# Performance work log

Hardware: AMD Instinct MI355X
Metric: run time of the kernel (lower is better)

## Reference

```python
import jax, jax.numpy as jnp
import numpy as np

RES = 192      # resolution
RANK = 8       # low-rank
FD = 32        # feature_dim
NFPD = 32      # num_features_per_dim = round(32768**(1/3))
RADIUS = 1.3
NI = 128       # n_intersections
STEP = 0.0352  # step_size
B = 2048       # rays


def setup_inputs():
    key = jax.random.key(0)
    ks = jax.random.split(key, 12)
    ro = jax.random.normal(ks[0], (B, 3), dtype=jnp.float32)
    ro = ro / jnp.linalg.norm(ro, axis=-1, keepdims=True) * 2.5  # origins outside the cube
    rd = -ro + 0.1 * jax.random.normal(ks[1], (B, 3), dtype=jnp.float32)
    rd = rd / jnp.linalg.norm(rd, axis=-1, keepdims=True)        # roughly toward origin
    def nrm(k, shape, std):
        return std * jax.random.normal(k, shape, dtype=jnp.float32)
    return {
        "rays_o": ro, "rays_d": rd,
        "Gxy": nrm(ks[2], (RES, RES, 3, RANK), 0.1),
        "Gxz": nrm(ks[3], (RES, RES, 3, RANK), 0.1),
        "Gyz": nrm(ks[4], (RES, RES, 3, RANK), 0.1),
        "F_grid": nrm(ks[5], (NFPD, NFPD, NFPD, FD), 0.05),
        "sW0": nrm(ks[6], (FD, 128), FD ** -0.5),
        "sW1": nrm(ks[7], (128, 128), 128 ** -0.5),
        "sW2": nrm(ks[8], (128, 16), 128 ** -0.5),
        "cW0": nrm(ks[9], (31, 64), 31 ** -0.5),
        "cW1": nrm(ks[10], (64, 64), 64 ** -0.5),
        "cW2": nrm(ks[11], (64, 3), 64 ** -0.5),
    }


def trilinear(vol, coords):
    # vol: [D,H,W,C]; coords: [N,3] as (x,y,z) in [-1,1]; x indexes W (last spatial dim)
    # matches torch grid_sample(align_corners=True, mode='bilinear', padding_mode='border')
    D, H, W, C = vol.shape
    def prep(c, size):
        idx = jnp.clip((c + 1.0) * 0.5 * (size - 1), 0.0, size - 1.0)  # border clamp
        i0 = jnp.clip(jnp.floor(idx).astype(jnp.int32), 0, size - 2)
        return i0, i0 + 1, idx - i0
    x0, x1, wx = prep(coords[:, 0], W)
    y0, y1, wy = prep(coords[:, 1], H)
    z0, z1, wz = prep(coords[:, 2], D)
    wx = wx[:, None]; wy = wy[:, None]; wz = wz[:, None]
    def g(zi, yi, xi):
        return vol[zi, yi, xi]  # [N,C]
    c00 = g(z0, y0, x0) * (1 - wx) + g(z0, y0, x1) * wx
    c01 = g(z0, y1, x0) * (1 - wx) + g(z0, y1, x1) * wx
    c10 = g(z1, y0, x0) * (1 - wx) + g(z1, y0, x1) * wx
    c11 = g(z1, y1, x0) * (1 - wx) + g(z1, y1, x1) * wx
    c0 = c00 * (1 - wy) + c01 * wy
    c1 = c10 * (1 - wy) + c11 * wy
    return c0 * (1 - wz) + c1 * wz


def sh16(d):
    # tcnn SphericalHarmonics degree 4 on directions (input (d+1)/2 is unmapped back to d internally)
    x, y, z = d[:, 0], d[:, 1], d[:, 2]
    x2, y2, z2 = x * x, y * y, z * z
    return jnp.stack([
        jnp.full_like(x, 0.28209479177387814),
        -0.48860251190291987 * y,
        0.48860251190291987 * z,
        -0.48860251190291987 * x,
        1.0925484305920792 * x * y,
        -1.0925484305920792 * y * z,
        0.94617469575755997 * z2 - 0.31539156525251999,
        -1.0925484305920792 * x * z,
        0.54627421529603959 * (x2 - y2),
        0.59004358992664352 * y * (-3.0 * x2 + y2),
        2.8906114426405538 * x * y * z,
        0.45704579946446572 * y * (1.0 - 5.0 * z2),
        0.3731763325901154 * z * (5.0 * z2 - 3.0),
        0.45704579946446572 * x * (1.0 - 5.0 * z2),
        1.445305721320277 * z * (x2 - y2),
        0.59004358992664352 * x * (-x2 + 3.0 * y2),
    ], axis=-1)


def _forward(rays_o, rays_d, Gxy, Gxz, Gyz, F_grid, sW0, sW1, sW2, cW0, cW1, cW2):
    b = rays_o.shape[0]
    # --- get_intersections: ray/AABB [-R,R]^3, uniform marching ---
    d = jnp.where(jnp.abs(rays_d) < 1e-9, 1e-9, rays_d)
    t1 = (-RADIUS - rays_o) / d
    t2 = (RADIUS - rays_o) / d
    tmin = jnp.max(jnp.minimum(t1, t2), axis=-1)
    tmax = jnp.min(jnp.maximum(t1, t2), axis=-1)
    near = jnp.maximum(tmin, 0.0)
    ts = near[:, None] + jnp.arange(NI + 1, dtype=jnp.float32) * STEP  # intersections [B,NI+1]
    tmid = 0.5 * (ts[:, :-1] + ts[:, 1:])                              # [B,NI]
    pts = rays_o[:, None, :] + tmid[..., None] * rays_d[:, None, :]    # [B,NI,3]
    mask = (jnp.all(jnp.abs(pts) <= RADIUS, axis=-1)
            & (tmid <= tmax[:, None]) & (tmax > tmin)[:, None])        # [B,NI]
    rdn = rays_d / jnp.linalg.norm(rays_d, axis=-1, keepdims=True)
    # coordinate chain of forward + eval_pts nets out to pts/RADIUS in [-1,1]
    p = ((pts / RADIUS + 1.0) * RES / 2.0) * 2.0 / RES - 1.0
    pf = p.reshape(-1, 3)
    # --- densify low-rank tri-plane grid: sum_r Gxy*Gxz*Gyz -> [RES,RES,RES,3] ---
    grid = jnp.zeros((RES, RES, RES, 3), dtype=Gxy.dtype)
    for r in range(RANK):  # fixed small rank; avoids a [RES^3,3,RANK] intermediate
        grid = grid + (Gxy[:, :, None, :, r] * Gxz[:, None, :, :, r] * Gyz[None, :, :, :, r])
    # --- eval_pts: grid_sample -> hash-feature grid_sample -> MLPs ---
    Gvals = trilinear(grid, pf)            # [N,3]
    Fvals = trilinear(F_grid, Gvals)       # [N,FD]
    h = jax.nn.relu(Fvals @ sW0)
    h = jax.nn.relu(h @ sW1)
    out16 = h @ sW2                        # [N,16]
    sigma = out16[:, 0].reshape(b, NI)
    sigma = jax.nn.relu(jnp.where(mask, sigma, 0.0))
    rdn_pts = jnp.broadcast_to(rdn[:, None, :], (b, NI, 3)).reshape(-1, 3)
    ci = jnp.concatenate([sh16(rdn_pts), out16[:, 1:]], axis=-1)  # [N,31]
    c = jax.nn.relu(ci @ cW0)
    c = jax.nn.relu(c @ cW1)
    color = (c @ cW2).reshape(b, NI, 3)
    color = jnp.where(mask[..., None], color, 0.0)
    # --- sigma2alpha + shrgb2rgb (white background) ---
    dists = ts[:, 1:] - ts[:, :-1]         # |rdn| == 1
    alpha = 1.0 - jnp.exp(-sigma * dists)
    T = jnp.cumprod(1.0 - alpha + 1e-10, axis=-1)
    T = jnp.concatenate([jnp.ones_like(T[:, :1]), T[:, :-1]], axis=-1)  # exclusive
    w = alpha * T                          # abs_light [B,NI]
    rgb = jax.nn.sigmoid(color)
    acc = jnp.sum(w, axis=-1)
    return jnp.sum(w[..., None] * rgb, axis=1) + (1.0 - acc)[..., None]  # [B,3]


def reference(rays_o, rays_d, Gxy, Gxz, Gyz, F_grid, sW0, sW1, sW2, cW0, cW1, cW2):
    return _forward(rays_o, rays_d, Gxy, Gxz, Gyz, F_grid, sW0, sW1, sW2, cW0, cW1, cW2)
```

## Files before the change

kernel.cpp:

```cpp
#include <hip/hip_runtime.h>
#include <math.h>

#define RES 192
#define RANK 8
#define NI 128
#define LW 136

typedef __attribute__((ext_vector_type(8))) _Float16 h8;
typedef __attribute__((ext_vector_type(2))) _Float16 h2f;
typedef __attribute__((ext_vector_type(4))) float floatx4;

#define OFF_SW0 0
#define OFF_SW1 4096
#define OFF_SW2 20480
#define OFF_CW0 22528
#define OFF_CW1 24576
#define OFF_CW2 28672
#define PACK_TOTAL 29696

#define TRI_CELLS (RES*RES)
#define TRI_TOTAL (3*TRI_CELLS*24)
#define FG_TOTAL  (32*32*32*32)
#define PREP_TOTAL (PACK_TOTAL + TRI_TOTAL + FG_TOTAL)

__device__ __forceinline__ void prep_idx(float c, int size, int& i0, float& f){
    float idx = (c + 1.0f)*0.5f*(float)(size-1);
    idx = fminf(fmaxf(idx, 0.0f), (float)(size-1));
    int ii = (int)idx;
    if (ii > size-2) ii = size-2;
    i0 = ii;
    f = idx - (float)ii;
}

__device__ __forceinline__ float wred64(float v){
    #pragma unroll
    for (int o=32;o>0;o>>=1) v += __shfl_down(v, o, 64);
    return v;
}

__device__ __forceinline__ h8 shx1(h8 v){
    union { h8 h; int i[4]; } u; u.h = v;
    #pragma unroll
    for (int k=0;k<4;k++) u.i[k] = __shfl_xor(u.i[k], 1, 64);
    return u.h;
}

__global__ void __launch_bounds__(256) prep_all(
    const float* __restrict__ sW0, const float* __restrict__ sW1,
    const float* __restrict__ sW2, const float* __restrict__ cW0,
    const float* __restrict__ cW1, const float* __restrict__ cW2,
    const float* __restrict__ Gxy, const float* __restrict__ Gxz,
    const float* __restrict__ Gyz, const float* __restrict__ F_grid,
    _Float16* __restrict__ Wp, _Float16* __restrict__ Gp, _Float16* __restrict__ Fg)
{
    int e = blockIdx.x*256 + threadIdx.x;
    if (e < PACK_TOTAL){
        const float* src; int K, N, ksteps, base;
        if      (e < OFF_SW1){ src=sW0; K=32;  N=128; ksteps=1; base=OFF_SW0; }
        else if (e < OFF_SW2){ src=sW1; K=128; N=128; ksteps=4; base=OFF_SW1; }
        else if (e < OFF_CW0){ src=sW2; K=128; N=16;  ksteps=4; base=OFF_SW2; }
        else if (e < OFF_CW1){ src=cW0; K=31;  N=64;  ksteps=1; base=OFF_CW0; }
        else if (e < OFF_CW2){ src=cW1; K=64;  N=64;  ksteps=2; base=OFF_CW1; }
        else                 { src=cW2; K=64;  N=3;   ksteps=2; base=OFF_CW2; }
        int i = e - base;
        int j = i & 7, lane = (i>>3)&63, t = i>>9;
        int ks = t % ksteps, nt = t / ksteps;
        int k = ks*32 + (lane>>4)*8 + j;
        int n = nt*16 + (lane&15);
        float v = (k < K && n < N) ? src[k*N + n] : 0.0f;
        Wp[e] = (_Float16)v;
        return;
    }
    int e2 = e - PACK_TOTAL;
    if (e2 < TRI_TOTAL){
        int p    = e2 / (TRI_CELLS*24);
        int rem  = e2 - p*(TRI_CELLS*24);
        int cell = rem / 24;
        int c    = rem - cell*24;
        const float* src = (p==0) ? Gxy : (p==1) ? Gxz : Gyz;
        Gp[((size_t)(p*TRI_CELLS + cell))*32 + c] = (_Float16)src[(size_t)cell*24 + c];
        return;
    }
    int e3 = e2 - TRI_TOTAL;
    Fg[e3] = (_Float16)F_grid[e3];
}

__launch_bounds__(256, 4)
__global__ void nerf_fused(
    const float* __restrict__ rays_o, const float* __restrict__ rays_d,
    const _Float16* __restrict__ Gp, const _Float16* __restrict__ Fg,
    const _Float16* __restrict__ Wp, float* __restrict__ out)
{
    __shared__ _Float16 buf[128*LW];
    __shared__ float sigmaArr[128];
    __shared__ float rgbArr[128*3];
    __shared__ float wtot[2];
    __shared__ float partial[8];

    const int tid  = threadIdx.x;
    const int lane = tid & 63;
    const int wv   = tid >> 6;
    const int ray  = blockIdx.x;

    const int rowbase = wv*32;
    const int col  = lane & 15;
    const int quad = lane >> 4;
    const int ar0  = rowbase + col;
    const int ar1  = ar0 + 16;

    const float ox = rays_o[ray*3+0], oy = rays_o[ray*3+1], oz = rays_o[ray*3+2];
    const float dx = rays_d[ray*3+0], dy = rays_d[ray*3+1], dz = rays_d[ray*3+2];

    float sdx = (fabsf(dx) < 1e-9f) ? 1e-9f : dx;
    float sdy = (fabsf(dy) < 1e-9f) ? 1e-9f : dy;
    float sdz = (fabsf(dz) < 1e-9f) ? 1e-9f : dz;
    float t1x = (-1.3f - ox)/sdx, t2x = (1.3f - ox)/sdx;
    float t1y = (-1.3f - oy)/sdy, t2y = (1.3f - oy)/sdy;
    float t1z = (-1.3f - oz)/sdz, t2z = (1.3f - oz)/sdz;
    float tmin = fmaxf(fminf(t1x,t2x), fmaxf(fminf(t1y,t2y), fminf(t1z,t2z)));
    float tmax = fminf(fmaxf(t1x,t2x), fminf(fmaxf(t1y,t2y), fmaxf(t1z,t2z)));
    float nearv = fmaxf(tmin, 0.0f);

    bool skipAll;
    {
        int sid = rowbase + (lane & 31);
        float w_ts0 = nearv + (float)sid     * 0.0352f;
        float w_ts1 = nearv + (float)(sid+1) * 0.0352f;
        float w_tm  = 0.5f*(w_ts0+w_ts1);
        float wpx = ox + w_tm*dx, wpy = oy + w_tm*dy, wpz = oz + w_tm*dz;
        bool m = (fabsf(wpx)<=1.3f) && (fabsf(wpy)<=1.3f) && (fabsf(wpz)<=1.3f)
               && (w_tm<=tmax) && (tmax>tmin);
        skipAll = (__ballot(m) == 0ULL);
    }

    if (!skipAll){
        {
            const int s = rowbase + (lane >> 1);
            const int h = lane & 1;

            float ts0 = nearv + (float)s     * 0.0352f;
            float ts1 = nearv + (float)(s+1) * 0.0352f;
            float tmid = 0.5f*(ts0+ts1);
            float px = ox + tmid*dx, py = oy + tmid*dy, pz = oz + tmid*dz;
            bool mask = (fabsf(px)<=1.3f) && (fabsf(py)<=1.3f) && (fabsf(pz)<=1.3f)
                      && (tmid<=tmax) && (tmax>tmin);

            h8 FVa = {0,0,0,0,0,0,0,0};
            h8 FVb = {0,0,0,0,0,0,0,0};

            if (mask){
                float p0 = (px/1.3f + 1.0f)*192.0f/2.0f*2.0f/192.0f - 1.0f;
                float p1 = (py/1.3f + 1.0f)*192.0f/2.0f*2.0f/192.0f - 1.0f;
                float p2 = (pz/1.3f + 1.0f)*192.0f/2.0f*2.0f/192.0f - 1.0f;

                int x0, y0, z0; float fx, fy, fz;
                prep_idx(p0, RES, x0, fx);
                prep_idx(p1, RES, y0, fy);
                prep_idx(p2, RES, z0, fz);

                const int zi  = z0 + h;
                const float wzc = h ? fz : (1.0f - fz);
                const int yiA = y0 + h;
                const int yiB = y0 + 1 - h;

                h8 XYA[3], XYB[3], XZ0[3], XZ1[3], YZo0[3], YZo1[3];
                {
                    const h8* pxyA = (const h8*)(Gp + ((size_t)(zi*RES + yiA))*32);
                    const h8* pxyB = (const h8*)(Gp + ((size_t)(zi*RES + yiB))*32);
                    const h8* px0  = (const h8*)(Gp + ((size_t)(TRI_CELLS + zi*RES + x0  ))*32);
                    const h8* px1  = (const h8*)(Gp + ((size_t)(TRI_CELLS + zi*RES + x0+1))*32);
                    const h8* py0  = (const h8*)(Gp + ((size_t)(2*TRI_CELLS + yiA*RES + x0  ))*32);
                    const h8* py1  = (const h8*)(Gp + ((size_t)(2*TRI_CELLS + yiA*RES + x0+1))*32);
                    #pragma unroll
                    for (int q=0;q<3;q++){
                        XYA[q]=pxyA[q]; XYB[q]=pxyB[q];
                        XZ0[q]=px0[q];  XZ1[q]=px1[q];
                        YZo0[q]=py0[q]; YZo1[q]=py1[q];
                    }
                }
                h8 YZp0[3], YZp1[3];
                #pragma unroll
                for (int q=0;q<3;q++){ YZp0[q]=shx1(YZo0[q]); YZp1[q]=shx1(YZo1[q]); }

                const float wyA = h ? fy : (1.0f - fy);
                const float wyB = h ? (1.0f - fy) : fy;

                h8 ACC0 = {0,0,0,0,0,0,0,0};
                h8 ACC1 = {0,0,0,0,0,0,0,0};
                h8 ACC2 = {0,0,0,0,0,0,0,0};
                #pragma unroll
                for (int yo=0; yo<2; yo++){
                    const float wy = yo ? wyB : wyA;
                    #pragma unroll
                    for (int xc=0; xc<2; xc++){
                        const float wx = xc ? fx : (1.0f - fx);
                        const _Float16 wh = (_Float16)(wzc*wy*wx);
                        const h8 w8 = {wh,wh,wh,wh,wh,wh,wh,wh};
                        h8 Q0, Q1, Q2;
                        if (yo==0){
                            const h8* YZv = xc ? YZo1 : YZo0;
                            Q0 = (XYA[0]*(xc?XZ1[0]:XZ0[0]))*YZv[0];
                            Q1 = (XYA[1]*(xc?XZ1[1]:XZ0[1]))*YZv[1];
                            Q2 = (XYA[2]*(xc?XZ1[2]:XZ0[2]))*YZv[2];
                        } else {
                            const h8* YZv = xc ? YZp1 : YZp0;
                            Q0 = (XYB[0]*(xc?XZ1[0]:XZ0[0]))*YZv[0];
                            Q1 = (XYB[1]*(xc?XZ1[1]:XZ0[1]))*YZv[1];
                            Q2 = (XYB[2]*(xc?XZ1[2]:XZ0[2]))*YZv[2];
                        }
                        ACC0 = __builtin_elementwise_fma(Q0, w8, ACC0);
                        ACC1 = __builtin_elementwise_fma(Q1, w8, ACC1);
                        ACC2 = __builtin_elementwise_fma(Q2, w8, ACC2);
                    }
                }
                h2f a0h = __builtin_shufflevector(ACC0,ACC0,0,1) + __builtin_shufflevector(ACC0,ACC0,2,3);
                h2f b0h = __builtin_shufflevector(ACC0,ACC0,4,5) + __builtin_shufflevector(ACC0,ACC0,6,7);
                h2f c0h = a0h + b0h;
                float gv0 = (float)c0h[0] + (float)c0h[1];
                h2f a1h = __builtin_shufflevector(ACC1,ACC1,0,1) + __builtin_shufflevector(ACC1,ACC1,2,3);
                h2f b1h = __builtin_shufflevector(ACC1,ACC1,4,5) + __builtin_shufflevector(ACC1,ACC1,6,7);
                h2f c1h = a1h + b1h;
                float gv1 = (float)c1h[0] + (float)c1h[1];
                h2f a2h = __builtin_shufflevector(ACC2,ACC2,0,1) + __builtin_shufflevector(ACC2,ACC2,2,3);
                h2f b2h = __builtin_shufflevector(ACC2,ACC2,4,5) + __builtin_shufflevector(ACC2,ACC2,6,7);
                h2f c2h = a2h + b2h;
                float gv2 = (float)c2h[0] + (float)c2h[1];

                gv0 += __shfl_xor(gv0, 1, 64);
                gv1 += __shfl_xor(gv1, 1, 64);
                gv2 += __shfl_xor(gv2, 1, 64);

                int a0,b0,c0; float fa,fb,fc;
                prep_idx(gv2, 32, a0, fa);
                prep_idx(gv1, 32, b0, fb);
                prep_idx(gv0, 32, c0, fc);
                #pragma unroll
                for (int zc=0; zc<2; zc++){
                    const int zi2 = a0+zc; const float wz2 = zc ? fa : 1.f-fa;
                    #pragma unroll
                    for (int yc=0; yc<2; yc++){
                        const int yi2 = b0+yc; const float wy2 = yc ? fb : 1.f-fb;
                        #pragma unroll
                        for (int xc=0; xc<2; xc++){
                            const int xi2 = c0+xc; const float wx2 = xc ? fc : 1.f-fc;
                            const _Float16 wh = (_Float16)(wz2*wy2*wx2);
                            const h8 w8 = {wh,wh,wh,wh,wh,wh,wh,wh};
                            const h8* pf = (const h8*)(Fg + ((size_t)((zi2*32+yi2)*32+xi2))*32 + h*16);
                            FVa = __builtin_elementwise_fma(pf[0], w8, FVa);
                            FVb = __builtin_elementwise_fma(pf[1], w8, FVb);
                        }
                    }
                }
            }

            *(h8*)&buf[s*LW + h*16]     = FVa;
            *(h8*)&buf[s*LW + h*16 + 8] = FVb;
        }

        {
            h8 a0 = *(const h8*)&buf[ar0*LW + quad*8];
            h8 a1 = *(const h8*)&buf[ar1*LW + quad*8];
            const h8* W = (const h8*)(Wp + OFF_SW0);
            #pragma unroll
            for (int nt=0; nt<8; nt++){
                h8 b = W[nt*64 + lane];
                floatx4 c0v = {0.f,0.f,0.f,0.f}, c1v = {0.f,0.f,0.f,0.f};
                c0v = __builtin_amdgcn_mfma_f32_16x16x32_f16(a0, b, c0v, 0,0,0);
                c1v = __builtin_amdgcn_mfma_f32_16x16x32_f16(a1, b, c1v, 0,0,0);
                #pragma unroll
                for (int r=0;r<4;r++){
                    int row0 = rowbase + quad*4 + r;
                    buf[row0*LW      + nt*16 + col] = (_Float16)fmaxf(c0v[r],0.f);
                    buf[(row0+16)*LW + nt*16 + col] = (_Float16)fmaxf(c1v[r],0.f);
                }
            }
        }

        {
            h8 A0[4], A1[4];
            #pragma unroll
            for (int ks=0;ks<4;ks++){
                A0[ks] = *(const h8*)&buf[ar0*LW + ks*32 + quad*8];
                A1[ks] = *(const h8*)&buf[ar1*LW + ks*32 + quad*8];
            }
            const h8* W = (const h8*)(Wp + OFF_SW1);
            #pragma unroll
            for (int nt=0; nt<8; nt++){
                floatx4 c0v = {0.f,0.f,0.f,0.f}, c1v = {0.f,0.f,0.f,0.f};
                #pragma unroll
                for (int ks=0;ks<4;ks++){
                    h8 b = W[(nt*4+ks)*64 + lane];
                    c0v = __builtin_amdgcn_mfma_f32_16x16x32_f16(A0[ks], b, c0v, 0,0,0);
                    c1v = __builtin_amdgcn_mfma_f32_16x16x32_f16(A1[ks], b, c1v, 0,0,0);
                }
                #pragma unroll
                for (int r=0;r<4;r++){
                    int row0 = rowbase + quad*4 + r;
                    buf[row0*LW      + nt*16 + col] = (_Float16)fmaxf(c0v[r],0.f);
                    buf[(row0+16)*LW + nt*16 + col] = (_Float16)fmaxf(c1v[r],0.f);
                }
            }
        }

        {
            h8 A0[4], A1[4];
            #pragma unroll
            for (int ks=0;ks<4;ks++){
                A0[ks] = *(const h8*)&buf[ar0*LW + ks*32 + quad*8];
                A1[ks] = *(const h8*)&buf[ar1*LW + ks*32 + quad*8];
            }
            const h8* W = (const h8*)(Wp + OFF_SW2);
            floatx4 c0v = {0.f,0.f,0.f,0.f}, c1v = {0.f,0.f,0.f,0.f};
            #pragma unroll
            for (int ks=0;ks<4;ks++){
                h8 b = W[ks*64 + lane];
                c0v = __builtin_amdgcn_mfma_f32_16x16x32_f16(A0[ks], b, c0v, 0,0,0);
                c1v = __builtin_amdgcn_mfma_f32_16x16x32_f16(A1[ks], b, c1v, 0,0,0);
            }
            #pragma unroll
            for (int r=0;r<4;r++){
                int row0 = rowbase + quad*4 + r;
                if (col == 0){
                    sigmaArr[row0]    = c0v[r];
                    sigmaArr[row0+16] = c1v[r];
                } else {
                    buf[row0*LW      + 15 + col] = (_Float16)c0v[r];
                    buf[(row0+16)*LW + 15 + col] = (_Float16)c1v[r];
                }
            }
            const float dn = sqrtf(dx*dx+dy*dy+dz*dz);
            const float X = dx/dn, Y = dy/dn, Z = dz/dn;
            const float X2=X*X, Y2=Y*Y, Z2=Z*Z;
            float sh[16];
            sh[0]= 0.28209479177387814f;
            sh[1]=-0.48860251190291987f*Y;
            sh[2]= 0.48860251190291987f*Z;
            sh[3]=-0.48860251190291987f*X;
            sh[4]= 1.0925484305920792f*X*Y;
            sh[5]=-1.0925484305920792f*Y*Z;
            sh[6]= 0.94617469575756f*Z2 - 0.31539156525252f;
            sh[7]=-1.0925484305920792f*X*Z;
            sh[8]= 0.5462742152960396f*(X2-Y2);
            sh[9]= 0.5900435899266435f*Y*(-3.0f*X2+Y2);
            sh[10]=2.890611442640554f*X*Y*Z;
            sh[11]=0.4570457994644657f*Y*(1.0f-5.0f*Z2);
            sh[12]=0.3731763325901154f*Z*(5.0f*Z2-3.0f);
            sh[13]=0.4570457994644657f*X*(1.0f-5.0f*Z2);
            sh[14]=1.445305721320277f*Z*(X2-Y2);
            sh[15]=0.5900435899266435f*X*(-X2+3.0f*Y2);
            if (lane < 32){
                int row = rowbase + lane;
                #pragma unroll
                for (int k=0;k<16;k++) buf[row*LW + k] = (_Float16)sh[k];
            }
        }

        {
            h8 a0 = *(const h8*)&buf[ar0*LW + quad*8];
            h8 a1 = *(const h8*)&buf[ar1*LW + quad*8];
            const h8* W = (const h8*)(Wp + OFF_CW0);
            #pragma unroll
            for (int nt=0; nt<4; nt++){
                h8 b = W[nt*64 + lane];
                floatx4 c0v = {0.f,0.f,0.f,0.f}, c1v = {0.f,0.f,0.f,0.f};
                c0v = __builtin_amdgcn_mfma_f32_16x16x32_f16(a0, b, c0v, 0,0,0);
                c1v = __builtin_amdgcn_mfma_f32_16x16x32_f16(a1, b, c1v, 0,0,0);
                #pragma unroll
                for (int r=0;r<4;r++){
                    int row0 = rowbase + quad*4 + r;
                    buf[row0*LW      + nt*16 + col] = (_Float16)fmaxf(c0v[r],0.f);
                    buf[(row0+16)*LW + nt*16 + col] = (_Float16)fmaxf(c1v[r],0.f);
                }
            }
        }

        {
            h8 A0[2], A1[2];
            #pragma unroll
            for (int ks=0;ks<2;ks++){
                A0[ks] = *(const h8*)&buf[ar0*LW + ks*32 + quad*8];
                A1[ks] = *(const h8*)&buf[ar1*LW + ks*32 + quad*8];
            }
            const h8* W = (const h8*)(Wp + OFF_CW1);
            #pragma unroll
            for (int nt=0; nt<4; nt++){
                floatx4 c0v = {0.f,0.f,0.f,0.f}, c1v = {0.f,0.f,0.f,0.f};
                #pragma unroll
                for (int ks=0;ks<2;ks++){
                    h8 b = W[(nt*2+ks)*64 + lane];
                    c0v = __builtin_amdgcn_mfma_f32_16x16x32_f16(A0[ks], b, c0v, 0,0,0);
                    c1v = __builtin_amdgcn_mfma_f32_16x16x32_f16(A1[ks], b, c1v, 0,0,0);
                }
                #pragma unroll
                for (int r=0;r<4;r++){
                    int row0 = rowbase + quad*4 + r;
                    buf[row0*LW      + nt*16 + col] = (_Float16)fmaxf(c0v[r],0.f);
                    buf[(row0+16)*LW + nt*16 + col] = (_Float16)fmaxf(c1v[r],0.f);
                }
            }
        }

        {
            h8 A0[2], A1[2];
            #pragma unroll
            for (int ks=0;ks<2;ks++){
                A0[ks] = *(const h8*)&buf[ar0*LW + ks*32 + quad*8];
                A1[ks] = *(const h8*)&buf[ar1*LW + ks*32 + quad*8];
            }
            const h8* W = (const h8*)(Wp + OFF_CW2);
            floatx4 c0v = {0.f,0.f,0.f,0.f}, c1v = {0.f,0.f,0.f,0.f};
            #pragma unroll
            for (int ks=0;ks<2;ks++){
                h8 b = W[ks*64 + lane];
                c0v = __builtin_amdgcn_mfma_f32_16x16x32_f16(A0[ks], b, c0v, 0,0,0);
                c1v = __builtin_amdgcn_mfma_f32_16x16x32_f16(A1[ks], b, c1v, 0,0,0);
            }
            if (col < 3){
                #pragma unroll
                for (int r=0;r<4;r++){
                    int row0 = rowbase + quad*4 + r;
                    rgbArr[row0*3 + col]      = c0v[r];
                    rgbArr[(row0+16)*3 + col] = c1v[r];
                }
            }
        }
    }

    __syncthreads();

    {
        float alpha = 0.f, rr = 0.f, rg = 0.f, rb = 0.f;
        if (tid < 128){
            float ts0 = nearv + (float)tid     * 0.0352f;
            float ts1 = nearv + (float)(tid+1) * 0.0352f;
            float tmid = 0.5f*(ts0+ts1);
            float dist = ts1 - ts0;
            float px = ox + tmid*dx, py = oy + tmid*dy, pz = oz + tmid*dz;
            bool mask = (fabsf(px)<=1.3f) && (fabsf(py)<=1.3f) && (fabsf(pz)<=1.3f)
                      && (tmid<=tmax) && (tmax>tmin);
            float sg = mask ? fmaxf(sigmaArr[tid], 0.f) : 0.f;
            alpha = 1.0f - expf(-sg*dist);
            if (mask){
                rr = 1.0f/(1.0f+expf(-rgbArr[tid*3+0]));
                rg = 1.0f/(1.0f+expf(-rgbArr[tid*3+1]));
                rb = 1.0f/(1.0f+expf(-rgbArr[tid*3+2]));
            }
        }
        float p = 1.0f - alpha + 1e-10f;
        #pragma unroll
        for (int off=1; off<64; off<<=1){
            float u = __shfl_up(p, off, 64);
            if (lane >= off) p *= u;
        }
        if (tid < 128 && lane == 63) wtot[wv] = p;
        float excl = __shfl_up(p, 1, 64);
        if (lane == 0) excl = 1.0f;
        __syncthreads();
        if (tid < 128){
            float T = excl;
            if (wv == 1) T *= wtot[0];
            float w = alpha * T;
            float v0 = wred64(w*rr);
            float v1 = wred64(w*rg);
            float v2 = wred64(w*rb);
            float v3 = wred64(w);
            if (lane == 0){
                partial[wv*4+0]=v0; partial[wv*4+1]=v1; partial[wv*4+2]=v2; partial[wv*4+3]=v3;
            }
        }
        __syncthreads();
        if (tid == 0){
            float acc = partial[3] + partial[7];
            float bg  = 1.0f - acc;
            out[ray*3+0] = partial[0] + partial[4] + bg;
            out[ray*3+1] = partial[1] + partial[5] + bg;
            out[ray*3+2] = partial[2] + partial[6] + bg;
        }
    }
}

extern "C" void kernel_launch(void* const* d_in, const int* in_sizes, int n_in,
                              void* d_out, int out_size, void* d_ws, size_t ws_size,
                              hipStream_t stream){
    const float* rays_o = (const float*)d_in[0];
    const float* rays_d = (const float*)d_in[1];
    const float* Gxy    = (const float*)d_in[2];
    const float* Gxz    = (const float*)d_in[3];
    const float* Gyz    = (const float*)d_in[4];
    const float* F_grid = (const float*)d_in[5];
    const float* sW0    = (const float*)d_in[6];
    const float* sW1    = (const float*)d_in[7];
    const float* sW2    = (const float*)d_in[8];
    const float* cW0    = (const float*)d_in[9];
    const float* cW1    = (const float*)d_in[10];
    const float* cW2    = (const float*)d_in[11];

    _Float16* Wp = (_Float16*)d_ws;
    _Float16* Gp = Wp + PACK_TOTAL;
    _Float16* Fg = Gp + (size_t)3*TRI_CELLS*32;

    prep_all<<<PREP_TOTAL/256, 256, 0, stream>>>(sW0,sW1,sW2,cW0,cW1,cW2,
                                                 Gxy,Gxz,Gyz,F_grid, Wp,Gp,Fg);
    nerf_fused<<<2048, 256, 0, stream>>>(rays_o, rays_d, Gp, Fg, Wp, (float*)d_out);
}
```

Baseline: 130.7 us.

## Split rays into half-blocks, add separate composite kernel, vectorize weight prep

The fused per-ray kernel is split so each ray is handled by two 128-thread blocks of 64 samples each. Each half exits early on its own when none of its samples fall inside the volume. Per-sample sigma and color go to a workspace buffer, and a new composite kernel does alpha compositing with one wave per ray. The prep kernel now converts factor planes and the feature grid with float4 loads and h8 stores instead of one scalar per thread. The trade-offs are an extra kernel launch and a global round trip for the per-sample outputs.

```diff
diff --git a/kernel.cpp b/kernel.cpp
--- a/kernel.cpp
+++ b/kernel.cpp
@@ -19,9 +19,9 @@
 #define PACK_TOTAL 29696
 
 #define TRI_CELLS (RES*RES)
-#define TRI_TOTAL (3*TRI_CELLS*24)
+#define CELLS3    (3*TRI_CELLS)
 #define FG_TOTAL  (32*32*32*32)
-#define PREP_TOTAL (PACK_TOTAL + TRI_TOTAL + FG_TOTAL)
+#define PREP2_TOTAL (PACK_TOTAL + CELLS3 + FG_TOTAL/8)
 
 __device__ __forceinline__ void prep_idx(float c, int size, int& i0, float& f){
     float idx = (c + 1.0f)*0.5f*(float)(size-1);
@@ -45,7 +45,7 @@
     return u.h;
 }
 
-__global__ void __launch_bounds__(256) prep_all(
+__global__ void __launch_bounds__(256) prep_all2(
     const float* __restrict__ sW0, const float* __restrict__ sW1,
     const float* __restrict__ sW2, const float* __restrict__ cW0,
     const float* __restrict__ cW1, const float* __restrict__ cW2,
@@ -72,35 +72,47 @@
         return;
     }
     int e2 = e - PACK_TOTAL;
-    if (e2 < TRI_TOTAL){
-        int p    = e2 / (TRI_CELLS*24);
-        int rem  = e2 - p*(TRI_CELLS*24);
-        int cell = rem / 24;
-        int c    = rem - cell*24;
-        const float* src = (p==0) ? Gxy : (p==1) ? Gxz : Gyz;
-        Gp[((size_t)(p*TRI_CELLS + cell))*32 + c] = (_Float16)src[(size_t)cell*24 + c];
+    if (e2 < CELLS3){
+        int p, lc;
+        if      (e2 < TRI_CELLS)   { p = 0; lc = e2; }
+        else if (e2 < 2*TRI_CELLS) { p = 1; lc = e2 - TRI_CELLS; }
+        else                       { p = 2; lc = e2 - 2*TRI_CELLS; }
+        const float* src = ((p==0) ? Gxy : (p==1) ? Gxz : Gyz) + (size_t)lc*24;
+        const float4* s4 = (const float4*)src;
+        float4 a = s4[0], b = s4[1], c = s4[2], d = s4[3], ee = s4[4], ff = s4[5];
+        h8 o0 = {(_Float16)a.x,(_Float16)a.y,(_Float16)a.z,(_Float16)a.w,
+                 (_Float16)b.x,(_Float16)b.y,(_Float16)b.z,(_Float16)b.w};
+        h8 o1 = {(_Float16)c.x,(_Float16)c.y,(_Float16)c.z,(_Float16)c.w,
+                 (_Float16)d.x,(_Float16)d.y,(_Float16)d.z,(_Float16)d.w};
+        h8 o2 = {(_Float16)ee.x,(_Float16)ee.y,(_Float16)ee.z,(_Float16)ee.w,
+                 (_Float16)ff.x,(_Float16)ff.y,(_Float16)ff.z,(_Float16)ff.w};
+        h8 zz = {0,0,0,0,0,0,0,0};
+        h8* dst = (h8*)(Gp + (size_t)e2*32);
+        dst[0]=o0; dst[1]=o1; dst[2]=o2; dst[3]=zz;
         return;
     }
-    int e3 = e2 - TRI_TOTAL;
-    Fg[e3] = (_Float16)F_grid[e3];
-}
-
-__launch_bounds__(256, 4)
-__global__ void nerf_fused(
+    int t = e2 - CELLS3;
+    const float4* s4 = (const float4*)(F_grid + (size_t)t*8);
+    float4 a = s4[0], b = s4[1];
+    h8 o = {(_Float16)a.x,(_Float16)a.y,(_Float16)a.z,(_Float16)a.w,
+            (_Float16)b.x,(_Float16)b.y,(_Float16)b.z,(_Float16)b.w};
+    ((h8*)Fg)[t] = o;
+}
+
+__launch_bounds__(128, 4)
+__global__ void nerf_half(
     const float* __restrict__ rays_o, const float* __restrict__ rays_d,
     const _Float16* __restrict__ Gp, const _Float16* __restrict__ Fg,
-    const _Float16* __restrict__ Wp, float* __restrict__ out)
+    const _Float16* __restrict__ Wp, float* __restrict__ SO)
 {
-    __shared__ _Float16 buf[128*LW];
-    __shared__ float sigmaArr[128];
-    __shared__ float rgbArr[128*3];
-    __shared__ float wtot[2];
-    __shared__ float partial[8];
+    __shared__ _Float16 buf[64*LW];
 
     const int tid  = threadIdx.x;
     const int lane = tid & 63;
     const int wv   = tid >> 6;
-    const int ray  = blockIdx.x;
+    const int ray  = blockIdx.x >> 1;
+    const int half = blockIdx.x & 1;
+    const int base = half*64;
 
     const int rowbase = wv*32;
     const int col  = lane & 15;
@@ -123,7 +135,7 @@
 
     bool skipAll;
     {
-        int sid = rowbase + (lane & 31);
+        int sid = base + rowbase + (lane & 31);
         float w_ts0 = nearv + (float)sid     * 0.0352f;
         float w_ts1 = nearv + (float)(sid+1) * 0.0352f;
         float w_tm  = 0.5f*(w_ts0+w_ts1);
@@ -132,350 +144,366 @@
                && (w_tm<=tmax) && (tmax>tmin);
         skipAll = (__ballot(m) == 0ULL);
     }
-
-    if (!skipAll){
-        {
-            const int s = rowbase + (lane >> 1);
-            const int h = lane & 1;
-
-            float ts0 = nearv + (float)s     * 0.0352f;
-            float ts1 = nearv + (float)(s+1) * 0.0352f;
-            float tmid = 0.5f*(ts0+ts1);
-            float px = ox + tmid*dx, py = oy + tmid*dy, pz = oz + tmid*dz;
-            bool mask = (fabsf(px)<=1.3f) && (fabsf(py)<=1.3f) && (fabsf(pz)<=1.3f)
-                      && (tmid<=tmax) && (tmax>tmin);
-
-            h8 FVa = {0,0,0,0,0,0,0,0};
-            h8 FVb = {0,0,0,0,0,0,0,0};
-
-            if (mask){
-                float p0 = (px/1.3f + 1.0f)*192.0f/2.0f*2.0f/192.0f - 1.0f;
-                float p1 = (py/1.3f + 1.0f)*192.0f/2.0f*2.0f/192.0f - 1.0f;
-                float p2 = (pz/1.3f + 1.0f)*192.0f/2.0f*2.0f/192.0f - 1.0f;
-
-                int x0, y0, z0; float fx, fy, fz;
-                prep_idx(p0, RES, x0, fx);
-                prep_idx(p1, RES, y0, fy);
-                prep_idx(p2, RES, z0, fz);
-
-                const int zi  = z0 + h;
-                const float wzc = h ? fz : (1.0f - fz);
-                const int yiA = y0 + h;
-                const int yiB = y0 + 1 - h;
-
-                h8 XYA[3], XYB[3], XZ0[3], XZ1[3], YZo0[3], YZo1[3];
-                {
-                    const h8* pxyA = (const h8*)(Gp + ((size_t)(zi*RES + yiA))*32);
-                    const h8* pxyB = (const h8*)(Gp + ((size_t)(zi*RES + yiB))*32);
-                    const h8* px0  = (const h8*)(Gp + ((size_t)(TRI_CELLS + zi*RES + x0  ))*32);
-                    const h8* px1  = (const h8*)(Gp + ((size_t)(TRI_CELLS + zi*RES + x0+1))*32);
-                    const h8* py0  = (const h8*)(Gp + ((size_t)(2*TRI_CELLS + yiA*RES + x0  ))*32);
-                    const h8* py1  = (const h8*)(Gp + ((size_t)(2*TRI_CELLS + yiA*RES + x0+1))*32);
+    if (skipAll) return;
+
+    {
+        const int s_loc = rowbase + (lane >> 1);
+        const int s_glb = base + s_loc;
+        const int h = lane & 1;
+
+        float ts0 = nearv + (float)s_glb     * 0.0352f;
+        float ts1 = nearv + (float)(s_glb+1) * 0.0352f;
+        float tmid = 0.5f*(ts0+ts1);
+        float px = ox + tmid*dx, py = oy + tmid*dy, pz = oz + tmid*dz;
+        bool mask = (fabsf(px)<=1.3f) && (fabsf(py)<=1.3f) && (fabsf(pz)<=1.3f)
+                  && (tmid<=tmax) && (tmax>tmin);
+
+        h8 FVa = {0,0,0,0,0,0,0,0};
+        h8 FVb = {0,0,0,0,0,0,0,0};
+
+        if (mask){
+            float p0 = (px/1.3f + 1.0f)*192.0f/2.0f*2.0f/192.0f - 1.0f;
+            float p1 = (py/1.3f + 1.0f)*192.0f/2.0f*2.0f/192.0f - 1.0f;
+            float p2 = (pz/1.3f + 1.0f)*192.0f/2.0f*2.0f/192.0f - 1.0f;
+
+            int x0, y0, z0; float fx, fy, fz;
+            prep_idx(p0, RES, x0, fx);
+            prep_idx(p1, RES, y0, fy);
+            prep_idx(p2, RES, z0, fz);
+
+            const int zi  = z0 + h;
+            const float wzc = h ? fz : (1.0f - fz);
+            const int yiA = y0 + h;
+            const int yiB = y0 + 1 - h;
+
+            h8 XYA[3], XYB[3], XZ0[3], XZ1[3], YZo0[3], YZo1[3];
+            {
+                const h8* pxyA = (const h8*)(Gp + ((size_t)(zi*RES + yiA))*32);
+                const h8* pxyB = (const h8*)(Gp + ((size_t)(zi*RES + yiB))*32);
+                const h8* px0  = (const h8*)(Gp + ((size_t)(TRI_CELLS + zi*RES + x0  ))*32);
+                const h8* px1  = (const h8*)(Gp + ((size_t)(TRI_CELLS + zi*RES + x0+1))*32);
+                const h8* py0  = (const h8*)(Gp + ((size_t)(2*TRI_CELLS + yiA*RES + x0  ))*32);
+                const h8* py1  = (const h8*)(Gp + ((size_t)(2*TRI_CELLS + yiA*RES + x0+1))*32);
+                #pragma unroll
+                for (int q=0;q<3;q++){
+                    XYA[q]=pxyA[q]; XYB[q]=pxyB[q];
+                    XZ0[q]=px0[q];  XZ1[q]=px1[q];
+                    YZo0[q]=py0[q]; YZo1[q]=py1[q];
+                }
+            }
+            h8 YZp0[3], YZp1[3];
+            #pragma unroll
+            for (int q=0;q<3;q++){ YZp0[q]=shx1(YZo0[q]); YZp1[q]=shx1(YZo1[q]); }
+
+            const float wyA = h ? fy : (1.0f - fy);
+            const float wyB = h ? (1.0f - fy) : fy;
+
+            h8 ACC0 = {0,0,0,0,0,0,0,0};
+            h8 ACC1 = {0,0,0,0,0,0,0,0};
+            h8 ACC2 = {0,0,0,0,0,0,0,0};
+            #pragma unroll
+            for (int yo=0; yo<2; yo++){
+                const float wy = yo ? wyB : wyA;
+                #pragma unroll
+                for (int xc=0; xc<2; xc++){
+                    const float wx = xc ? fx : (1.0f - fx);
+                    const _Float16 wh = (_Float16)(wzc*wy*wx);
+                    const h8 w8 = {wh,wh,wh,wh,wh,wh,wh,wh};
+                    h8 Q0, Q1, Q2;
+                    if (yo==0){
+                        const h8* YZv = xc ? YZo1 : YZo0;
+                        Q0 = (XYA[0]*(xc?XZ1[0]:XZ0[0]))*YZv[0];
+                        Q1 = (XYA[1]*(xc?XZ1[1]:XZ0[1]))*YZv[1];
+                        Q2 = (XYA[2]*(xc?XZ1[2]:XZ0[2]))*YZv[2];
+                    } else {
+                        const h8* YZv = xc ? YZp1 : YZp0;
+                        Q0 = (XYB[0]*(xc?XZ1[0]:XZ0[0]))*YZv[0];
+                        Q1 = (XYB[1]*(xc?XZ1[1]:XZ0[1]))*YZv[1];
+                        Q2 = (XYB[2]*(xc?XZ1[2]:XZ0[2]))*YZv[2];
+                    }
+                    ACC0 = __builtin_elementwise_fma(Q0, w8, ACC0);
+                    ACC1 = __builtin_elementwise_fma(Q1, w8, ACC1);
+                    ACC2 = __builtin_elementwise_fma(Q2, w8, ACC2);
+                }
+            }
+            h2f a0h = __builtin_shufflevector(ACC0,ACC0,0,1) + __builtin_shufflevector(ACC0,ACC0,2,3);
+            h2f b0h = __builtin_shufflevector(ACC0,ACC0,4,5) + __builtin_shufflevector(ACC0,ACC0,6,7);
+            h2f c0h = a0h + b0h;
+            float gv0 = (float)c0h[0] + (float)c0h[1];
+            h2f a1h = __builtin_shufflevector(ACC1,ACC1,0,1) + __builtin_shufflevector(ACC1,ACC1,2,3);
+            h2f b1h = __builtin_shufflevector(ACC1,ACC1,4,5) + __builtin_shufflevector(ACC1,ACC1,6,7);
+            h2f c1h = a1h + b1h;
+            float gv1 = (float)c1h[0] + (float)c1h[1];
+            h2f a2h = __builtin_shufflevector(ACC2,ACC2,0,1) + __builtin_shufflevector(ACC2,ACC2,2,3);
+            h2f b2h = __builtin_shufflevector(ACC2,ACC2,4,5) + __builtin_shufflevector(ACC2,ACC2,6,7);
+            h2f c2h = a2h + b2h;
+            float gv2 = (float)c2h[0] + (float)c2h[1];
+
+            gv0 += __shfl_xor(gv0, 1, 64);
+            gv1 += __shfl_xor(gv1, 1, 64);
+            gv2 += __shfl_xor(gv2, 1, 64);
+
+            int a0,b0,c0; float fa,fb,fc;
+            prep_idx(gv2, 32, a0, fa);
+            prep_idx(gv1, 32, b0, fb);
+            prep_idx(gv0, 32, c0, fc);
+            #pragma unroll
+            for (int zc=0; zc<2; zc++){
+                const int zi2 = a0+zc; const float wz2 = zc ? fa : 1.f-fa;
+                #pragma unroll
+                for (int yc=0; yc<2; yc++){
+                    const int yi2 = b0+yc; const float wy2 = yc ? fb : 1.f-fb;
                     #pragma unroll
-                    for (int q=0;q<3;q++){
-                        XYA[q]=pxyA[q]; XYB[q]=pxyB[q];
-                        XZ0[q]=px0[q];  XZ1[q]=px1[q];
-                        YZo0[q]=py0[q]; YZo1[q]=py1[q];
+                    for (int xc=0; xc<2; xc++){
+                        const int xi2 = c0+xc; const float wx2 = xc ? fc : 1.f-fc;
+                        const _Float16 wh = (_Float16)(wz2*wy2*wx2);
+                        const h8 w8 = {wh,wh,wh,wh,wh,wh,wh,wh};
+                        const h8* pf = (const h8*)(Fg + ((size_t)((zi2*32+yi2)*32+xi2))*32 + h*16);
+                        FVa = __builtin_elementwise_fma(pf[0], w8, FVa);
+                        FVb = __builtin_elementwise_fma(pf[1], w8, FVb);
                     }
                 }
-                h8 YZp0[3], YZp1[3];
-                #pragma unroll
-                for (int q=0;q<3;q++){ YZp0[q]=shx1(YZo0[q]); YZp1[q]=shx1(YZo1[q]); }
-
-                const float wyA = h ? fy : (1.0f - fy);
-                const float wyB = h ? (1.0f - fy) : fy;
-
-                h8 ACC0 = {0,0,0,0,0,0,0,0};
-                h8 ACC1 = {0,0,0,0,0,0,0,0};
-                h8 ACC2 = {0,0,0,0,0,0,0,0};
-                #pragma unroll
-                for (int yo=0; yo<2; yo++){
-                    const float wy = yo ? wyB : wyA;
-                    #pragma unroll
-                    for (int xc=0; xc<2; xc++){
-                        const float wx = xc ? fx : (1.0f - fx);
-                        const _Float16 wh = (_Float16)(wzc*wy*wx);
-                        const h8 w8 = {wh,wh,wh,wh,wh,wh,wh,wh};
-                        h8 Q0, Q1, Q2;
-                        if (yo==0){
-                            const h8* YZv = xc ? YZo1 : YZo0;
-                            Q0 = (XYA[0]*(xc?XZ1[0]:XZ0[0]))*YZv[0];
-                            Q1 = (XYA[1]*(xc?XZ1[1]:XZ0[1]))*YZv[1];
-                            Q2 = (XYA[2]*(xc?XZ1[2]:XZ0[2]))*YZv[2];
-                        } else {
-                            const h8* YZv = xc ? YZp1 : YZp0;
-                            Q0 = (XYB[0]*(xc?XZ1[0]:XZ0[0]))*YZv[0];
-                            Q1 = (XYB[1]*(xc?XZ1[1]:XZ0[1]))*YZv[1];
-                            Q2 = (XYB[2]*(xc?XZ1[2]:XZ0[2]))*YZv[2];
-                        }
-                        ACC0 = __builtin_elementwise_fma(Q0, w8, ACC0);
-                        ACC1 = __builtin_elementwise_fma(Q1, w8, ACC1);
-                        ACC2 = __builtin_elementwise_fma(Q2, w8, ACC2);
-                    }
-                }
-                h2f a0h = __builtin_shufflevector(ACC0,ACC0,0,1) + __builtin_shufflevector(ACC0,ACC0,2,3);
-                h2f b0h = __builtin_shufflevector(ACC0,ACC0,4,5) + __builtin_shufflevector(ACC0,ACC0,6,7);
-                h2f c0h = a0h + b0h;
-                float gv0 = (float)c0h[0] + (float)c0h[1];
-                h2f a1h = __builtin_shufflevector(ACC1,ACC1,0,1) + __builtin_shufflevector(ACC1,ACC1,2,3);
-                h2f b1h = __builtin_shufflevector(ACC1,ACC1,4,5) + __builtin_shufflevector(ACC1,ACC1,6,7);
-                h2f c1h = a1h + b1h;
-                float gv1 = (float)c1h[0] + (float)c1h[1];
-                h2f a2h = __builtin_shufflevector(ACC2,ACC2,0,1) + __builtin_shufflevector(ACC2,ACC2,2,3);
-                h2f b2h = __builtin_shufflevector(ACC2,ACC2,4,5) + __builtin_shufflevector(ACC2,ACC2,6,7);
-                h2f c2h = a2h + b2h;
-                float gv2 = (float)c2h[0] + (float)c2h[1];
-
-                gv0 += __shfl_xor(gv0, 1, 64);
-                gv1 += __shfl_xor(gv1, 1, 64);
-                gv2 += __shfl_xor(gv2, 1, 64);
-
-                int a0,b0,c0; float fa,fb,fc;
-                prep_idx(gv2, 32, a0, fa);
-                prep_idx(gv1, 32, b0, fb);
-                prep_idx(gv0, 32, c0, fc);
-                #pragma unroll
-                for (int zc=0; zc<2; zc++){
-                    const int zi2 = a0+zc; const float wz2 = zc ? fa : 1.f-fa;
-                    #pragma unroll
-                    for (int yc=0; yc<2; yc++){
-                        const int yi2 = b0+yc; const float wy2 = yc ? fb : 1.f-fb;
-                        #pragma unroll
-                        for (int xc=0; xc<2; xc++){
-                            const int xi2 = c0+xc; const float wx2 = xc ? fc : 1.f-fc;
-                            const _Float16 wh = (_Float16)(wz2*wy2*wx2);
-                            const h8 w8 = {wh,wh,wh,wh,wh,wh,wh,wh};
-                            const h8* pf = (const h8*)(Fg + ((size_t)((zi2*32+yi2)*32+xi2))*32 + h*16);
-                            FVa = __builtin_elementwise_fma(pf[0], w8, FVa);
-                            FVb = __builtin_elementwise_fma(pf[1], w8, FVb);
-                        }
-                    }
-                }
-            }
-
-            *(h8*)&buf[s*LW + h*16]     = FVa;
-            *(h8*)&buf[s*LW + h*16 + 8] = FVb;
-        }
-
-        {
-            h8 a0 = *(const h8*)&buf[ar0*LW + quad*8];
-            h8 a1 = *(const h8*)&buf[ar1*LW + quad*8];
-            const h8* W = (const h8*)(Wp + OFF_SW0);
-            #pragma unroll
-            for (int nt=0; nt<8; nt++){
-                h8 b = W[nt*64 + lane];
-                floatx4 c0v = {0.f,0.f,0.f,0.f}, c1v = {0.f,0.f,0.f,0.f};
-                c0v = __builtin_amdgcn_mfma_f32_16x16x32_f16(a0, b, c0v, 0,0,0);
-                c1v = __builtin_amdgcn_mfma_f32_16x16x32_f16(a1, b, c1v, 0,0,0);
-                #pragma unroll
-                for (int r=0;r<4;r++){
-                    int row0 = rowbase + quad*4 + r;
-                    buf[row0*LW      + nt*16 + col] = (_Float16)fmaxf(c0v[r],0.f);
-                    buf[(row0+16)*LW + nt*16 + col] = (_Float16)fmaxf(c1v[r],0.f);
-                }
-            }
-        }
-
-        {
-            h8 A0[4], A1[4];
+            }
+        }
+
+        *(h8*)&buf[s_loc*LW + h*16]     = FVa;
+        *(h8*)&buf[s_loc*LW + h*16 + 8] = FVb;
+    }
+
+    {
+        h8 a0 = *(const h8*)&buf[ar0*LW + quad*8];
+        h8 a1 = *(const h8*)&buf[ar1*LW + quad*8];
+        const h8* W = (const h8*)(Wp + OFF_SW0);
+        #pragma unroll
+        for (int nt=0; nt<8; nt++){
+            h8 b = W[nt*64 + lane];
+            floatx4 c0v = {0.f,0.f,0.f,0.f}, c1v = {0.f,0.f,0.f,0.f};
+            c0v = __builtin_amdgcn_mfma_f32_16x16x32_f16(a0, b, c0v, 0,0,0);
+            c1v = __builtin_amdgcn_mfma_f32_16x16x32_f16(a1, b, c1v, 0,0,0);
+            #pragma unroll
+            for (int r=0;r<4;r++){
+                int row0 = rowbase + quad*4 + r;
+                buf[row0*LW      + nt*16 + col] = (_Float16)fmaxf(c0v[r],0.f);
+                buf[(row0+16)*LW + nt*16 + col] = (_Float16)fmaxf(c1v[r],0.f);
+            }
+        }
+    }
+
+    {
+        h8 A0[4], A1[4];
+        #pragma unroll
+        for (int ks=0;ks<4;ks++){
+            A0[ks] = *(const h8*)&buf[ar0*LW + ks*32 + quad*8];
+            A1[ks] = *(const h8*)&buf[ar1*LW + ks*32 + quad*8];
+        }
+        const h8* W = (const h8*)(Wp + OFF_SW1);
+        #pragma unroll
+        for (int nt=0; nt<8; nt++){
+            floatx4 c0v = {0.f,0.f,0.f,0.f}, c1v = {0.f,0.f,0.f,0.f};
             #pragma unroll
             for (int ks=0;ks<4;ks++){
-                A0[ks] = *(const h8*)&buf[ar0*LW + ks*32 + quad*8];
-                A1[ks] = *(const h8*)&buf[ar1*LW + ks*32 + quad*8];
-            }
-            const h8* W = (const h8*)(Wp + OFF_SW1);
-            #pragma unroll
-            for (int nt=0; nt<8; nt++){
-                floatx4 c0v = {0.f,0.f,0.f,0.f}, c1v = {0.f,0.f,0.f,0.f};
-                #pragma unroll
-                for (int ks=0;ks<4;ks++){
-                    h8 b = W[(nt*4+ks)*64 + lane];
-                    c0v = __builtin_amdgcn_mfma_f32_16x16x32_f16(A0[ks], b, c0v, 0,0,0);
-                    c1v = __builtin_amdgcn_mfma_f32_16x16x32_f16(A1[ks], b, c1v, 0,0,0);
-                }
-                #pragma unroll
-                for (int r=0;r<4;r++){
-                    int row0 = rowbase + quad*4 + r;
-                    buf[row0*LW      + nt*16 + col] = (_Float16)fmaxf(c0v[r],0.f);
-                    buf[(row0+16)*LW + nt*16 + col] = (_Float16)fmaxf(c1v[r],0.f);
-                }
-            }
-        }
-
-        {
-            h8 A0[4], A1[4];
-            #pragma unroll
-            for (int ks=0;ks<4;ks++){
-                A0[ks] = *(const h8*)&buf[ar0*LW + ks*32 + quad*8];
-                A1[ks] = *(const h8*)&buf[ar1*LW + ks*32 + quad*8];
-            }
-            const h8* W = (const h8*)(Wp + OFF_SW2);
-            floatx4 c0v = {0.f,0.f,0.f,0.f}, c1v = {0.f,0.f,0.f,0.f};
-            #pragma unroll
-            for (int ks=0;ks<4;ks++){
-                h8 b = W[ks*64 + lane];
+                h8 b = W[(nt*4+ks)*64 + lane];
                 c0v = __builtin_amdgcn_mfma_f32_16x16x32_f16(A0[ks], b, c0v, 0,0,0);
                 c1v = __builtin_amdgcn_mfma_f32_16x16x32_f16(A1[ks], b, c1v, 0,0,0);
             }
             #pragma unroll
             for (int r=0;r<4;r++){
                 int row0 = rowbase + quad*4 + r;
-                if (col == 0){
-                    sigmaArr[row0]    = c0v[r];
-                    sigmaArr[row0+16] = c1v[r];
-                } else {
-                    buf[row0*LW      + 15 + col] = (_Float16)c0v[r];
-                    buf[(row0+16)*LW + 15 + col] = (_Float16)c1v[r];
-                }
-            }
-            const float dn = sqrtf(dx*dx+dy*dy+dz*dz);
-            const float X = dx/dn, Y = dy/dn, Z = dz/dn;
-            const float X2=X*X, Y2=Y*Y, Z2=Z*Z;
-            float sh[16];
-            sh[0]= 0.28209479177387814f;
-            sh[1]=-0.48860251190291987f*Y;
-            sh[2]= 0.48860251190291987f*Z;
-            sh[3]=-0.48860251190291987f*X;
-            sh[4]= 1.0925484305920792f*X*Y;
-            sh[5]=-1.0925484305920792f*Y*Z;
-            sh[6]= 0.94617469575756f*Z2 - 0.31539156525252f;
-            sh[7]=-1.0925484305920792f*X*Z;
-            sh[8]= 0.5462742152960396f*(X2-Y2);
-            sh[9]= 0.5900435899266435f*Y*(-3.0f*X2+Y2);
-            sh[10]=2.890611442640554f*X*Y*Z;
-            sh[11]=0.4570457994644657f*Y*(1.0f-5.0f*Z2);
-            sh[12]=0.3731763325901154f*Z*(5.0f*Z2-3.0f);
-            sh[13]=0.4570457994644657f*X*(1.0f-5.0f*Z2);
-            sh[14]=1.445305721320277f*Z*(X2-Y2);
-            sh[15]=0.5900435899266435f*X*(-X2+3.0f*Y2);
-            if (lane < 32){
-                int row = rowbase + lane;
-                #pragma unroll
-                for (int k=0;k<16;k++) buf[row*LW + k] = (_Float16)sh[k];
-            }
-        }
-
-        {
-            h8 a0 = *(const h8*)&buf[ar0*LW + quad*8];
-            h8 a1 = *(const h8*)&buf[ar1*LW + quad*8];
-            const h8* W = (const h8*)(Wp + OFF_CW0);
-            #pragma unroll
-            for (int nt=0; nt<4; nt++){
-                h8 b = W[nt*64 + lane];
-                floatx4 c0v = {0.f,0.f,0.f,0.f}, c1v = {0.f,0.f,0.f,0.f};
-                c0v = __builtin_amdgcn_mfma_f32_16x16x32_f16(a0, b, c0v, 0,0,0);
-                c1v = __builtin_amdgcn_mfma_f32_16x16x32_f16(a1, b, c1v, 0,0,0);
-                #pragma unroll
-                for (int r=0;r<4;r++){
-                    int row0 = rowbase + quad*4 + r;
-                    buf[row0*LW      + nt*16 + col] = (_Float16)fmaxf(c0v[r],0.f);
-                    buf[(row0+16)*LW + nt*16 + col] = (_Float16)fmaxf(c1v[r],0.f);
-                }
-            }
-        }
-
-        {
-            h8 A0[2], A1[2];
+                buf[row0*LW      + nt*16 + col] = (_Float16)fmaxf(c0v[r],0.f);
+                buf[(row0+16)*LW + nt*16 + col] = (_Float16)fmaxf(c1v[r],0.f);
+            }
+        }
+    }
+
+    {
+        h8 A0[4], A1[4];
+        #pragma unroll
+        for (int ks=0;ks<4;ks++){
+            A0[ks] = *(const h8*)&buf[ar0*LW + ks*32 + quad*8];
+            A1[ks] = *(const h8*)&buf[ar1*LW + ks*32 + quad*8];
+        }
+        const h8* W = (const h8*)(Wp + OFF_SW2);
+        floatx4 c0v = {0.f,0.f,0.f,0.f}, c1v = {0.f,0.f,0.f,0.f};
+        #pragma unroll
+        for (int ks=0;ks<4;ks++){
+            h8 b = W[ks*64 + lane];
+            c0v = __builtin_amdgcn_mfma_f32_16x16x32_f16(A0[ks], b, c0v, 0,0,0);
+            c1v = __builtin_amdgcn_mfma_f32_16x16x32_f16(A1[ks], b, c1v, 0,0,0);
+        }
+        #pragma unroll
+        for (int r=0;r<4;r++){
+            int row0 = rowbase + quad*4 + r;
+            if (col == 0){
+                int g0 = ray*128 + base + row0;
+                SO[(size_t)g0*4]      = c0v[r];
+                SO[(size_t)(g0+16)*4] = c1v[r];
+            } else {
+                buf[row0*LW      + 15 + col] = (_Float16)c0v[r];
+                buf[(row0+16)*LW + 15 + col] = (_Float16)c1v[r];
+            }
+        }
+        const float dn = sqrtf(dx*dx+dy*dy+dz*dz);
+        const float X = dx/dn, Y = dy/dn, Z = dz/dn;
+        const float X2=X*X, Y2=Y*Y, Z2=Z*Z;
+        float sh[16];
+        sh[0]= 0.28209479177387814f;
+        sh[1]=-0.48860251190291987f*Y;
+        sh[2]= 0.48860251190291987f*Z;
+        sh[3]=-0.48860251190291987f*X;
+        sh[4]= 1.0925484305920792f*X*Y;
+        sh[5]=-1.0925484305920792f*Y*Z;
+        sh[6]= 0.94617469575756f*Z2 - 0.31539156525252f;
+        sh[7]=-1.0925484305920792f*X*Z;
+        sh[8]= 0.5462742152960396f*(X2-Y2);
+        sh[9]= 0.5900435899266435f*Y*(-3.0f*X2+Y2);
+        sh[10]=2.890611442640554f*X*Y*Z;
+        sh[11]=0.4570457994644657f*Y*(1.0f-5.0f*Z2);
+        sh[12]=0.3731763325901154f*Z*(5.0f*Z2-3.0f);
+        sh[13]=0.4570457994644657f*X*(1.0f-5.0f*Z2);
+        sh[14]=1.445305721320277f*Z*(X2-Y2);
+        sh[15]=0.5900435899266435f*X*(-X2+3.0f*Y2);
+        if (lane < 32){
+            int row = rowbase + lane;
+            #pragma unroll
+            for (int k=0;k<16;k++) buf[row*LW + k] = (_Float16)sh[k];
+        }
+    }
+
+    {
+        h8 a0 = *(const h8*)&buf[ar0*LW + quad*8];
+        h8 a1 = *(const h8*)&buf[ar1*LW + quad*8];
+        const h8* W = (const h8*)(Wp + OFF_CW0);
+        #pragma unroll
+        for (int nt=0; nt<4; nt++){
+            h8 b = W[nt*64 + lane];
+            floatx4 c0v = {0.f,0.f,0.f,0.f}, c1v = {0.f,0.f,0.f,0.f};
+            c0v = __builtin_amdgcn_mfma_f32_16x16x32_f16(a0, b, c0v, 0,0,0);
+            c1v = __builtin_amdgcn_mfma_f32_16x16x32_f16(a1, b, c1v, 0,0,0);
+            #pragma unroll
+            for (int r=0;r<4;r++){
+                int row0 = rowbase + quad*4 + r;
+                buf[row0*LW      + nt*16 + col] = (_Float16)fmaxf(c0v[r],0.f);
+                buf[(row0+16)*LW + nt*16 + col] = (_Float16)fmaxf(c1v[r],0.f);
+            }
+        }
+    }
+
+    {
+        h8 A0[2], A1[2];
+        #pragma unroll
+        for (int ks=0;ks<2;ks++){
+            A0[ks] = *(const h8*)&buf[ar0*LW + ks*32 + quad*8];
+            A1[ks] = *(const h8*)&buf[ar1*LW + ks*32 + quad*8];
+        }
+        const h8* W = (const h8*)(Wp + OFF_CW1);
+        #pragma unroll
+        for (int nt=0; nt<4; nt++){
+            floatx4 c0v = {0.f,0.f,0.f,0.f}, c1v = {0.f,0.f,0.f,0.f};
             #pragma unroll
             for (int ks=0;ks<2;ks++){
-                A0[ks] = *(const h8*)&buf[ar0*LW + ks*32 + quad*8];
-                A1[ks] = *(const h8*)&buf[ar1*LW + ks*32 + quad*8];
-            }
-            const h8* W = (const h8*)(Wp + OFF_CW1);
-            #pragma unroll
-            for (int nt=0; nt<4; nt++){
-                floatx4 c0v = {0.f,0.f,0.f,0.f}, c1v = {0.f,0.f,0.f,0.f};
-                #pragma unroll
-                for (int ks=0;ks<2;ks++){
-                    h8 b = W[(nt*2+ks)*64 + lane];
-                    c0v = __builtin_amdgcn_mfma_f32_16x16x32_f16(A0[ks], b, c0v, 0,0,0);
-                    c1v = __builtin_amdgcn_mfma_f32_16x16x32_f16(A1[ks], b, c1v, 0,0,0);
-                }
-                #pragma unroll
-                for (int r=0;r<4;r++){
-                    int row0 = rowbase + quad*4 + r;
-                    buf[row0*LW      + nt*16 + col] = (_Float16)fmaxf(c0v[r],0.f);
-                    buf[(row0+16)*LW + nt*16 + col] = (_Float16)fmaxf(c1v[r],0.f);
-                }
-            }
-        }
-
-        {
-            h8 A0[2], A1[2];
-            #pragma unroll
-            for (int ks=0;ks<2;ks++){
-                A0[ks] = *(const h8*)&buf[ar0*LW + ks*32 + quad*8];
-                A1[ks] = *(const h8*)&buf[ar1*LW + ks*32 + quad*8];
-            }
-            const h8* W = (const h8*)(Wp + OFF_CW2);
-            floatx4 c0v = {0.f,0.f,0.f,0.f}, c1v = {0.f,0.f,0.f,0.f};
-            #pragma unroll
-            for (int ks=0;ks<2;ks++){
-                h8 b = W[ks*64 + lane];
+                h8 b = W[(nt*2+ks)*64 + lane];
                 c0v = __builtin_amdgcn_mfma_f32_16x16x32_f16(A0[ks], b, c0v, 0,0,0);
                 c1v = __builtin_amdgcn_mfma_f32_16x16x32_f16(A1[ks], b, c1v, 0,0,0);
             }
-            if (col < 3){
-                #pragma unroll
-                for (int r=0;r<4;r++){
-                    int row0 = rowbase + quad*4 + r;
-                    rgbArr[row0*3 + col]      = c0v[r];
-                    rgbArr[(row0+16)*3 + col] = c1v[r];
-                }
-            }
-        }
-    }
-
-    __syncthreads();
-
-    {
-        float alpha = 0.f, rr = 0.f, rg = 0.f, rb = 0.f;
-        if (tid < 128){
-            float ts0 = nearv + (float)tid     * 0.0352f;
-            float ts1 = nearv + (float)(tid+1) * 0.0352f;
-            float tmid = 0.5f*(ts0+ts1);
-            float dist = ts1 - ts0;
-            float px = ox + tmid*dx, py = oy + tmid*dy, pz = oz + tmid*dz;
-            bool mask = (fabsf(px)<=1.3f) && (fabsf(py)<=1.3f) && (fabsf(pz)<=1.3f)
-                      && (tmid<=tmax) && (tmax>tmin);
-            float sg = mask ? fmaxf(sigmaArr[tid], 0.f) : 0.f;
-            alpha = 1.0f - expf(-sg*dist);
-            if (mask){
-                rr = 1.0f/(1.0f+expf(-rgbArr[tid*3+0]));
-                rg = 1.0f/(1.0f+expf(-rgbArr[tid*3+1]));
-                rb = 1.0f/(1.0f+expf(-rgbArr[tid*3+2]));
-            }
-        }
-        float p = 1.0f - alpha + 1e-10f;
-        #pragma unroll
-        for (int off=1; off<64; off<<=1){
-            float u = __shfl_up(p, off, 64);
-            if (lane >= off) p *= u;
-        }
-        if (tid < 128 && lane == 63) wtot[wv] = p;
-        float excl = __shfl_up(p, 1, 64);
-        if (lane == 0) excl = 1.0f;
-        __syncthreads();
-        if (tid < 128){
-            float T = excl;
-            if (wv == 1) T *= wtot[0];
-            float w = alpha * T;
-            float v0 = wred64(w*rr);
-            float v1 = wred64(w*rg);
-            float v2 = wred64(w*rb);
-            float v3 = wred64(w);
-            if (lane == 0){
-                partial[wv*4+0]=v0; partial[wv*4+1]=v1; partial[wv*4+2]=v2; partial[wv*4+3]=v3;
-            }
-        }
-        __syncthreads();
-        if (tid == 0){
-            float acc = partial[3] + partial[7];
-            float bg  = 1.0f - acc;
-            out[ray*3+0] = partial[0] + partial[4] + bg;
-            out[ray*3+1] = partial[1] + partial[5] + bg;
-            out[ray*3+2] = partial[2] + partial[6] + bg;
-        }
+            #pragma unroll
+            for (int r=0;r<4;r++){
+                int row0 = rowbase + quad*4 + r;
+                buf[row0*LW      + nt*16 + col] = (_Float16)fmaxf(c0v[r],0.f);
+                buf[(row0+16)*LW + nt*16 + col] = (_Float16)fmaxf(c1v[r],0.f);
+            }
+        }
+    }
+
+    {
+        h8 A0[2], A1[2];
+        #pragma unroll
+        for (int ks=0;ks<2;ks++){
+            A0[ks] = *(const h8*)&buf[ar0*LW + ks*32 + quad*8];
+            A1[ks] = *(const h8*)&buf[ar1*LW + ks*32 + quad*8];
+        }
+        const h8* W = (const h8*)(Wp + OFF_CW2);
+        floatx4 c0v = {0.f,0.f,0.f,0.f}, c1v = {0.f,0.f,0.f,0.f};
+        #pragma unroll
+        for (int ks=0;ks<2;ks++){
+            h8 b = W[ks*64 + lane];
+            c0v = __builtin_amdgcn_mfma_f32_16x16x32_f16(A0[ks], b, c0v, 0,0,0);
+            c1v = __builtin_amdgcn_mfma_f32_16x16x32_f16(A1[ks], b, c1v, 0,0,0);
+        }
+        if (col < 3){
+            #pragma unroll
+            for (int r=0;r<4;r++){
+                int row0 = rowbase + quad*4 + r;
+                int g0 = ray*128 + base + row0;
+                SO[(size_t)g0*4      + 1 + col] = c0v[r];
+                SO[(size_t)(g0+16)*4 + 1 + col] = c1v[r];
+            }
+        }
+    }
+}
+
+__global__ void __launch_bounds__(256) composite(
+    const float* __restrict__ rays_o, const float* __restrict__ rays_d,
+    const float4* __restrict__ SO, float* __restrict__ out)
+{
+    const int lane = threadIdx.x & 63;
+    const int ray  = blockIdx.x*4 + (threadIdx.x >> 6);
+
+    const float ox = rays_o[ray*3+0], oy = rays_o[ray*3+1], oz = rays_o[ray*3+2];
+    const float dx = rays_d[ray*3+0], dy = rays_d[ray*3+1], dz = rays_d[ray*3+2];
+
+    float sdx = (fabsf(dx) < 1e-9f) ? 1e-9f : dx;
+    float sdy = (fabsf(dy) < 1e-9f) ? 1e-9f : dy;
+    float sdz = (fabsf(dz) < 1e-9f) ? 1e-9f : dz;
+    float t1x = (-1.3f - ox)/sdx, t2x = (1.3f - ox)/sdx;
+    float t1y = (-1.3f - oy)/sdy, t2y = (1.3f - oy)/sdy;
+    float t1z = (-1.3f - oz)/sdz, t2z = (1.3f - oz)/sdz;
+    float tmin = fmaxf(fminf(t1x,t2x), fmaxf(fminf(t1y,t2y), fminf(t1z,t2z)));
+    float tmax = fminf(fmaxf(t1x,t2x), fminf(fmaxf(t1y,t2y), fmaxf(t1z,t2z)));
+    float nearv = fmaxf(tmin, 0.0f);
+
+    float al[2], cr[2], cg[2], cb[2];
+    #pragma unroll
+    for (int k=0;k<2;k++){
+        int s = lane*2 + k;
+        float ts0 = nearv + (float)s     * 0.0352f;
+        float ts1 = nearv + (float)(s+1) * 0.0352f;
+        float tmid = 0.5f*(ts0+ts1);
+        float dist = ts1 - ts0;
+        float px = ox + tmid*dx, py = oy + tmid*dy, pz = oz + tmid*dz;
+        bool mask = (fabsf(px)<=1.3f) && (fabsf(py)<=1.3f) && (fabsf(pz)<=1.3f)
+                  && (tmid<=tmax) && (tmax>tmin);
+        float4 v = SO[(size_t)ray*128 + s];
+        float sg = mask ? fmaxf(v.x, 0.f) : 0.f;
+        al[k] = 1.0f - expf(-sg*dist);
+        if (mask){
+            cr[k] = 1.0f/(1.0f+expf(-v.y));
+            cg[k] = 1.0f/(1.0f+expf(-v.z));
+            cb[k] = 1.0f/(1.0f+expf(-v.w));
+        } else { cr[k]=0.f; cg[k]=0.f; cb[k]=0.f; }
+    }
+    float q0 = 1.0f - al[0] + 1e-10f;
+    float q1 = 1.0f - al[1] + 1e-10f;
+    float p = q0*q1;
+    #pragma unroll
+    for (int off=1; off<64; off<<=1){
+        float u = __shfl_up(p, off, 64);
+        if (lane >= off) p *= u;
+    }
+    float excl = __shfl_up(p, 1, 64);
+    if (lane == 0) excl = 1.0f;
+    float T0 = excl;
+    float T1 = excl*q0;
+    float w0 = al[0]*T0;
+    float w1 = al[1]*T1;
+    float v0 = wred64(w0*cr[0] + w1*cr[1]);
+    float v1 = wred64(w0*cg[0] + w1*cg[1]);
+    float v2 = wred64(w0*cb[0] + w1*cb[1]);
+    float v3 = wred64(w0 + w1);
+    if (lane == 0){
+        float bg = 1.0f - v3;
+        out[ray*3+0] = v0 + bg;
+        out[ray*3+1] = v1 + bg;
+        out[ray*3+2] = v2 + bg;
     }
 }
 
@@ -498,8 +526,10 @@
     _Float16* Wp = (_Float16*)d_ws;
     _Float16* Gp = Wp + PACK_TOTAL;
     _Float16* Fg = Gp + (size_t)3*TRI_CELLS*32;
-
-    prep_all<<<PREP_TOTAL/256, 256, 0, stream>>>(sW0,sW1,sW2,cW0,cW1,cW2,
-                                                 Gxy,Gxz,Gyz,F_grid, Wp,Gp,Fg);
-    nerf_fused<<<2048, 256, 0, stream>>>(rays_o, rays_d, Gp, Fg, Wp, (float*)d_out);
-}
+    float*    SO = (float*)(Fg + FG_TOTAL);
+
+    prep_all2<<<PREP2_TOTAL/256, 256, 0, stream>>>(sW0,sW1,sW2,cW0,cW1,cW2,
+                                                   Gxy,Gxz,Gyz,F_grid, Wp,Gp,Fg);
+    nerf_half<<<4096, 128, 0, stream>>>(rays_o, rays_d, Gp, Fg, Wp, SO);
+    composite<<<512, 256, 0, stream>>>(rays_o, rays_d, (const float4*)SO, (float*)d_out);
+}
```

After: 138.2 us. 1.06x slower.
